# Kernel tuning notes

Measured on AMD Instinct MI355X. Metric: run time of the kernel, lower is better.

Reference implementation:

```python
import jax, jax.numpy as jnp
import numpy as np

N = 50000
E = 800000
IN = 128
HID = 32
OUT = 32
H1, H2 = 4, 4
NEG_SLOPE = 0.2


def setup_inputs() -> dict:
    key = jax.random.key(0)
    ks = jax.random.split(key, 12)
    x = jax.random.normal(ks[0], (N, IN), dtype=jnp.float32)
    src = jax.random.randint(ks[1], (E,), 0, N, dtype=jnp.int32)
    dst = jax.random.randint(ks[2], (E,), 0, N, dtype=jnp.int32)
    s = 0.1
    # layer 1: fc (IN -> H1*HID, no bias), attn vectors (H1, HID), bias (H1*HID,)
    W1 = jax.random.normal(ks[3], (IN, H1 * HID), dtype=jnp.float32) * s
    al1 = jax.random.normal(ks[4], (H1, HID), dtype=jnp.float32) * s
    ar1 = jax.random.normal(ks[5], (H1, HID), dtype=jnp.float32) * s
    b1 = jnp.zeros((H1 * HID,), dtype=jnp.float32)
    # layer 2: fc (H1*HID -> H2*OUT, no bias)
    W2 = jax.random.normal(ks[6], (H1 * HID, H2 * OUT), dtype=jnp.float32) * s
    al2 = jax.random.normal(ks[7], (H2, OUT), dtype=jnp.float32) * s
    ar2 = jax.random.normal(ks[8], (H2, OUT), dtype=jnp.float32) * s
    b2 = jnp.zeros((H2 * OUT,), dtype=jnp.float32)
    return {"x": x, "W1": W1, "al1": al1, "ar1": ar1, "b1": b1,
            "W2": W2, "al2": al2, "ar2": ar2, "b2": b2,
            "src": src, "dst": dst}


def _gat_layer(x, W, al, ar, b, src, dst, n, h, d):
    # feat_drop is identity (eval mode)
    feat = (x @ W).reshape(n, h, d)                       # [N,H,D]
    el = jnp.einsum('nhd,hd->nh', feat, al)               # [N,H]
    er = jnp.einsum('nhd,hd->nh', feat, ar)               # [N,H]
    e = jax.nn.leaky_relu(el[src] + er[dst], NEG_SLOPE)   # [E,H] SDDMM
    # edge softmax over incoming edges of each destination node
    emax = jax.ops.segment_max(e, dst, num_segments=n)    # [N,H]
    emax = jnp.where(jnp.isfinite(emax), emax, 0.0)       # guard 0-in-degree
    w = jnp.exp(e - emax[dst])                            # [E,H]
    denom = jax.ops.segment_sum(w, dst, num_segments=n)   # [N,H]
    alpha = w / jnp.maximum(denom[dst], 1e-9)             # [E,H]; attn_drop identity
    # SpMM aggregation
    rst = jax.ops.segment_sum(feat[src] * alpha[:, :, None], dst, num_segments=n)
    # residual: in_feats == h*d for both layers -> DGL uses Identity res_fc
    rst = rst + x.reshape(n, h, d)
    rst = rst + b.reshape(1, h, d)
    return rst


def reference(x, W1, al1, ar1, b1, W2, al2, ar2, b2, src, dst):
    h = _gat_layer(x, W1, al1, ar1, b1, src, dst, N, H1, HID)
    h = jax.nn.elu(h)                                     # layer-1 activation
    h = h.reshape(N, H1 * HID)                            # flatten(1)
    h = _gat_layer(h, W2, al2, ar2, b2, src, dst, N, H2, OUT)
    return h.mean(axis=1)                                 # [N,OUT]
```

## Files before the change

### kernel.cpp

```cpp
#include <hip/hip_runtime.h>
#include <cstdint>
#include <cstddef>

#define NEG_SLOPE 0.2f

typedef __bf16 bf16x8 __attribute__((ext_vector_type(8)));
typedef float  f32x4  __attribute__((ext_vector_type(4)));

__device__ inline unsigned int bf16pair(float a, float b) {
    unsigned int ua = __float_as_uint(a), ub = __float_as_uint(b);
    ua += 0x7fffu + ((ua >> 16) & 1u);
    ub += 0x7fffu + ((ub >> 16) & 1u);
    return (ua >> 16) | (ub & 0xffff0000u);
}
__device__ inline unsigned short bf16r(float x) {
    unsigned int u = __float_as_uint(x);
    u += 0x7fffu + ((u >> 16) & 1u);
    return (unsigned short)(u >> 16);
}

__global__ __launch_bounds__(256) void wtrans_kernel(
    const float* __restrict__ W1, const float* __restrict__ W2,
    unsigned short* __restrict__ Wt1, unsigned short* __restrict__ Wt2)
{
    __shared__ float tile[64][65];
    const float* W = (blockIdx.x < 4) ? W1 : W2;
    unsigned short* Wt = (blockIdx.x < 4) ? Wt1 : Wt2;
    const int tb = blockIdx.x & 3;
    const int k0 = (tb >> 1) * 64, n0 = (tb & 1) * 64;
    const int c = threadIdx.x & 63, r4 = threadIdx.x >> 6;
#pragma unroll
    for (int i = 0; i < 16; ++i) {
        const int r = i * 4 + r4;
        tile[r][c] = W[(size_t)(k0 + r) * 128 + n0 + c];
    }
    __syncthreads();
#pragma unroll
    for (int i = 0; i < 16; ++i) {
        const int nn = i * 4 + r4;
        Wt[(size_t)(n0 + nn) * 128 + k0 + c] = bf16r(tile[c][nn]);
    }
}

__global__ __launch_bounds__(256, 3) void gemm_attn_kernel(
    const float* __restrict__ X, const unsigned short* __restrict__ Wt,
    const float* __restrict__ al, const float* __restrict__ ar,
    unsigned short* __restrict__ feat16, float* __restrict__ el,
    float* __restrict__ er, int n)
{
    __shared__ unsigned short sX[64][136];
    __shared__ unsigned short sW[128][136];

    const int t = threadIdx.x;
    const int rowbase = blockIdx.x * 64;

#pragma unroll
    for (int i = 0; i < 8; ++i) {
        const int idx = t + 256 * i;
        const int row = idx >> 5;
        const int kq  = (idx & 31) * 4;
        int g = rowbase + row; if (g >= n) g = n - 1;
        const float4 v = *(const float4*)&X[(size_t)g * 128 + kq];
        uint2 pk;
        pk.x = bf16pair(v.x, v.y);
        pk.y = bf16pair(v.z, v.w);
        *(uint2*)&sX[row][kq] = pk;
    }
#pragma unroll
    for (int i = 0; i < 8; ++i) {
        const int idx = t + 256 * i;
        const int row = idx >> 4;
        const int q   = idx & 15;
        *(uint4*)&sW[row][q * 8] = *(const uint4*)&Wt[(size_t)row * 128 + q * 8];
    }
    __syncthreads();

    const int lane = t & 63;
    const int w    = t >> 6;
    const int m    = lane & 15;
    const int g4   = lane >> 4;

    bf16x8 a[4];
#pragma unroll
    for (int ks = 0; ks < 4; ++ks)
        a[ks] = *(const bf16x8*)&sX[w * 16 + m][ks * 32 + g4 * 8];

    float elacc[4][4] = {{0}}, eracc[4][4] = {{0}};
    unsigned short fout[8][4];

#pragma unroll
    for (int ct = 0; ct < 8; ct += 2) {
        f32x4 acc0 = {0.f, 0.f, 0.f, 0.f}, acc1 = {0.f, 0.f, 0.f, 0.f};
        const int n0 = ct * 16 + m, n1 = n0 + 16;
#pragma unroll
        for (int ks = 0; ks < 4; ++ks) {
            const bf16x8 b0 = *(const bf16x8*)&sW[n0][ks * 32 + g4 * 8];
            const bf16x8 b1 = *(const bf16x8*)&sW[n1][ks * 32 + g4 * 8];
            acc0 = __builtin_amdgcn_mfma_f32_16x16x32_bf16(a[ks], b0, acc0, 0, 0, 0);
            acc1 = __builtin_amdgcn_mfma_f32_16x16x32_bf16(a[ks], b1, acc1, 0, 0, 0);
        }
        const int h = ct >> 1;
        const float al0 = al[n0], ar0 = ar[n0];
        const float al1 = al[n1], ar1 = ar[n1];
#pragma unroll
        for (int r = 0; r < 4; ++r) {
            elacc[r][h] += acc0[r] * al0 + acc1[r] * al1;
            eracc[r][h] += acc0[r] * ar0 + acc1[r] * ar1;
            fout[ct][r]     = bf16r(acc0[r]);
            fout[ct + 1][r] = bf16r(acc1[r]);
        }
    }

    __syncthreads();
#pragma unroll
    for (int ct = 0; ct < 8; ++ct)
#pragma unroll
        for (int r = 0; r < 4; ++r)
            sX[w * 16 + g4 * 4 + r][(ct & 1) * 16 + (ct >> 1) * 32 + m] = fout[ct][r];
    __syncthreads();
    {
        const int row = t >> 2;
        const int q   = t & 3;
        const int g   = rowbase + row;
        if (g < n) {
#pragma unroll
            for (int i = 0; i < 4; ++i) {
                const int c0 = q * 8 + i * 32;
                *(uint4*)&feat16[(size_t)g * 128 + c0] = *(const uint4*)&sX[row][c0];
            }
        }
    }

#pragma unroll
    for (int r = 0; r < 4; ++r)
#pragma unroll
        for (int h = 0; h < 4; ++h) {
            float a_ = elacc[r][h], b_ = eracc[r][h];
            a_ += __shfl_xor(a_, 1); b_ += __shfl_xor(b_, 1);
            a_ += __shfl_xor(a_, 2); b_ += __shfl_xor(b_, 2);
            a_ += __shfl_xor(a_, 4); b_ += __shfl_xor(b_, 4);
            a_ += __shfl_xor(a_, 8); b_ += __shfl_xor(b_, 8);
            elacc[r][h] = a_; eracc[r][h] = b_;
        }
    if (m == 0) {
#pragma unroll
        for (int r = 0; r < 4; ++r) {
            const int row = rowbase + w * 16 + g4 * 4 + r;
            if (row < n) {
#pragma unroll
                for (int h = 0; h < 4; ++h) {
                    el[(size_t)row * 4 + h] = elacc[r][h];
                    er[(size_t)row * 4 + h] = eracc[r][h];
                }
            }
        }
    }
}


__global__ void rank_kernel(const int* __restrict__ dst, int* __restrict__ deg,
                            int* __restrict__ rank, int E)
{
    const int e4 = (blockIdx.x * blockDim.x + threadIdx.x) * 4;
    if (e4 + 4 <= E) {
        const int4 d = *(const int4*)&dst[e4];
        int4 r;
        r.x = atomicAdd(&deg[d.x], 1);
        r.y = atomicAdd(&deg[d.y], 1);
        r.z = atomicAdd(&deg[d.z], 1);
        r.w = atomicAdd(&deg[d.w], 1);
        *(int4*)&rank[e4] = r;
    } else {
        for (int e = e4; e < E; ++e) rank[e] = atomicAdd(&deg[dst[e]], 1);
    }
}

__global__ __launch_bounds__(1024) void scan_kernel(
    const int* __restrict__ deg, int* __restrict__ off, int n)
{
    __shared__ int wsums[16];
    __shared__ int s_carry;
    const int tid  = threadIdx.x;
    const int lane = tid & 63;
    const int wid  = tid >> 6;

    if (tid == 0) { s_carry = 0; off[0] = 0; }
    __syncthreads();

    const int n4 = n >> 2;
    const int4* __restrict__ deg4 = (const int4*)deg;

    for (int base = 0; base < n4; base += 1024) {
        const int i4 = base + tid;
        int4 v = make_int4(0, 0, 0, 0);
        if (i4 < n4) v = deg4[i4];
        const int t0 = v.x, t1 = t0 + v.y, t2 = t1 + v.z, t3 = t2 + v.w;

        int x = t3;
#pragma unroll
        for (int d = 1; d < 64; d <<= 1) {
            int y = __shfl_up(x, d);
            if (lane >= d) x += y;
        }
        if (lane == 63) wsums[wid] = x;
        __syncthreads();

        if (wid == 0 && lane < 16) {
            int xx = wsums[lane];
#pragma unroll
            for (int d = 1; d < 16; d <<= 1) {
                int y = __shfl_up(xx, d);
                if (lane >= d) xx += y;
            }
            wsums[lane] = xx;
        }
        __syncthreads();

        const int wp   = (wid == 0) ? 0 : wsums[wid - 1];
        const int excl = s_carry + wp + (x - t3);
        if (i4 < n4) {
            off[4 * i4 + 1] = excl + t0;
            off[4 * i4 + 2] = excl + t1;
            off[4 * i4 + 3] = excl + t2;
            off[4 * i4 + 4] = excl + t3;
        }
        __syncthreads();
        if (tid == 0) s_carry += wsums[15];
        __syncthreads();
    }
}

__global__ void place_kernel(const int* __restrict__ src, const int* __restrict__ dst,
                             const int* __restrict__ off, const int* __restrict__ rank,
                             int* __restrict__ csr_src, int E)
{
    const int e4 = (blockIdx.x * blockDim.x + threadIdx.x) * 4;
    if (e4 + 4 <= E) {
        const int4 s = *(const int4*)&src[e4];
        const int4 d = *(const int4*)&dst[e4];
        const int4 r = *(const int4*)&rank[e4];
        const int o0 = off[d.x], o1 = off[d.y], o2 = off[d.z], o3 = off[d.w];
        csr_src[o0 + r.x] = s.x;
        csr_src[o1 + r.y] = s.y;
        csr_src[o2 + r.z] = s.z;
        csr_src[o3 + r.w] = s.w;
    } else {
        for (int e = e4; e < E; ++e)
            csr_src[off[dst[e]] + rank[e]] = src[e];
    }
}

template <bool LAYER2>
__global__ __launch_bounds__(256) void agg_kernel(
    const int* __restrict__ off, const int* __restrict__ csr_src,
    const unsigned short* __restrict__ feat16, const float* __restrict__ el,
    const float* __restrict__ er, const float* __restrict__ resid,
    const float* __restrict__ bias, float* __restrict__ out, int n)
{
    const int lane = threadIdx.x & 63;
    const int node = blockIdx.x * 4 + (threadIdx.x >> 6);
    if (node >= n) return;

    const int h  = lane >> 4;
    const int d0 = 2 * lane;

    const float erh = er[(size_t)node * 4 + h];
    const unsigned int* __restrict__ fb = (const unsigned int*)feat16;

    const int beg = off[node], end = off[node + 1];

    float acc0 = 0.f, acc1 = 0.f, sw = 0.f;
    int j = beg;

#define EDGE4(J)                                                              \
    {                                                                         \
        const int s0 = csr_src[J], s1 = csr_src[(J) + 1];                     \
        const int s2 = csr_src[(J) + 2], s3 = csr_src[(J) + 3];               \
        const float e0 = el[(size_t)s0 * 4 + h];                              \
        const float e1 = el[(size_t)s1 * 4 + h];                              \
        const float e2 = el[(size_t)s2 * 4 + h];                              \
        const float e3 = el[(size_t)s3 * 4 + h];                              \
        const unsigned int u0 = fb[(size_t)s0 * 64 + lane];                   \
        const unsigned int u1 = fb[(size_t)s1 * 64 + lane];                   \
        const unsigned int u2 = fb[(size_t)s2 * 64 + lane];                   \
        const unsigned int u3 = fb[(size_t)s3 * 64 + lane];                   \
        float a0 = e0 + erh, a1 = e1 + erh, a2 = e2 + erh, a3 = e3 + erh;     \
        a0 = (a0 >= 0.f) ? a0 : NEG_SLOPE * a0;                               \
        a1 = (a1 >= 0.f) ? a1 : NEG_SLOPE * a1;                               \
        a2 = (a2 >= 0.f) ? a2 : NEG_SLOPE * a2;                               \
        a3 = (a3 >= 0.f) ? a3 : NEG_SLOPE * a3;                               \
        const float w0 = __expf(a0), w1 = __expf(a1);                         \
        const float w2 = __expf(a2), w3 = __expf(a3);                         \
        acc0 += w0 * __uint_as_float(u0 << 16);                               \
        acc1 += w0 * __uint_as_float(u0 & 0xffff0000u);                       \
        acc0 += w1 * __uint_as_float(u1 << 16);                               \
        acc1 += w1 * __uint_as_float(u1 & 0xffff0000u);                       \
        acc0 += w2 * __uint_as_float(u2 << 16);                               \
        acc1 += w2 * __uint_as_float(u2 & 0xffff0000u);                       \
        acc0 += w3 * __uint_as_float(u3 << 16);                               \
        acc1 += w3 * __uint_as_float(u3 & 0xffff0000u);                       \
        sw += w0 + w1 + w2 + w3;                                              \
    }

    for (; j + 8 <= end; j += 8) { EDGE4(j) EDGE4(j + 4) }
    for (; j + 4 <= end; j += 4) { EDGE4(j) }
#undef EDGE4
    for (; j < end; ++j) {
        const int s = csr_src[j];
        float e = el[(size_t)s * 4 + h] + erh;
        e = (e >= 0.f) ? e : NEG_SLOPE * e;
        const float w = __expf(e);
        const unsigned int u = fb[(size_t)s * 64 + lane];
        acc0 += w * __uint_as_float(u << 16);
        acc1 += w * __uint_as_float(u & 0xffff0000u);
        sw += w;
    }

    const float inv = 1.f / fmaxf(sw, 1e-9f);
    const float2 rs = *(const float2*)&resid[(size_t)node * 128 + d0];
    float v0 = acc0 * inv + rs.x + bias[d0];
    float v1 = acc1 * inv + rs.y + bias[d0 + 1];

    if (!LAYER2) {
        v0 = (v0 > 0.f) ? v0 : expm1f(v0);
        v1 = (v1 > 0.f) ? v1 : expm1f(v1);
        *(float2*)&out[(size_t)node * 128 + d0] = make_float2(v0, v1);
    } else {
        float s0 = v0, s1 = v1;
        s0 += __shfl_xor(s0, 16); s1 += __shfl_xor(s1, 16);
        s0 += __shfl_xor(s0, 32); s1 += __shfl_xor(s1, 32);
        if (lane < 16)
            *(float2*)&out[(size_t)node * 32 + 2 * lane] =
                make_float2(s0 * 0.25f, s1 * 0.25f);
    }
}

extern "C" void kernel_launch(void* const* d_in, const int* in_sizes, int n_in,
                              void* d_out, int out_size, void* d_ws, size_t ws_size,
                              hipStream_t stream)
{
    const float* x   = (const float*)d_in[0];
    const float* W1  = (const float*)d_in[1];
    const float* al1 = (const float*)d_in[2];
    const float* ar1 = (const float*)d_in[3];
    const float* b1  = (const float*)d_in[4];
    const float* W2  = (const float*)d_in[5];
    const float* al2 = (const float*)d_in[6];
    const float* ar2 = (const float*)d_in[7];
    const float* b2  = (const float*)d_in[8];
    const int*   src = (const int*)d_in[9];
    const int*   dst = (const int*)d_in[10];

    const int n = in_sizes[0] / 128;
    const int E = in_sizes[9];
    float* out = (float*)d_out;

    char* p = (char*)d_ws;
    float* h1    = (float*)p;          p += (size_t)n * 128 * sizeof(float);
    unsigned short* feat16 = (unsigned short*)p; p += (size_t)n * 128 * sizeof(unsigned short);
    float* el    = (float*)p;          p += (size_t)n * 4 * sizeof(float);
    float* er    = (float*)p;          p += (size_t)n * 4 * sizeof(float);
    int* off     = (int*)p;            p += (size_t)(n + 1) * sizeof(int);
    int* deg     = (int*)p;            p += (size_t)n * sizeof(int);
    int* rank    = (int*)p;            p += (size_t)E * sizeof(int);
    int* csr     = (int*)p;            p += (size_t)E * sizeof(int);
    unsigned short* wt1 = (unsigned short*)p; p += (size_t)128 * 128 * sizeof(unsigned short);
    unsigned short* wt2 = (unsigned short*)p; p += (size_t)128 * 128 * sizeof(unsigned short);

    hipMemsetAsync(deg, 0, (size_t)n * sizeof(int), stream);

    const int gemm_grid  = (n + 63) / 64;
    const int edge4_grid = (E / 4 + 255) / 256;
    const int agg_grid   = (n + 3) / 4;

    wtrans_kernel<<<8, 256, 0, stream>>>(W1, W2, wt1, wt2);
    gemm_attn_kernel<<<gemm_grid, 256, 0, stream>>>(x, wt1, al1, ar1, feat16, el, er, n);
    rank_kernel<<<edge4_grid, 256, 0, stream>>>(dst, deg, rank, E);
    scan_kernel<<<1, 1024, 0, stream>>>(deg, off, n);
    place_kernel<<<edge4_grid, 256, 0, stream>>>(src, dst, off, rank, csr, E);
    agg_kernel<false><<<agg_grid, 256, 0, stream>>>(off, csr, feat16, el, er, x, b1, h1, n);
    gemm_attn_kernel<<<gemm_grid, 256, 0, stream>>>(h1, wt2, al2, ar2, feat16, el, er, n);
    agg_kernel<true><<<agg_grid, 256, 0, stream>>>(off, csr, feat16, el, er, h1, b2, out, n);
}
```

Baseline: 270.1 us.

## Fuse degree-rank pass into layer-1 GEMM launch and deepen aggregation gather batching

```diff
diff --git a/kernel.cpp b/kernel.cpp
--- a/kernel.cpp
+++ b/kernel.cpp
@@ -42,16 +42,37 @@
     }
 }
 
+template <bool RANK>
 __global__ __launch_bounds__(256, 3) void gemm_attn_kernel(
     const float* __restrict__ X, const unsigned short* __restrict__ Wt,
     const float* __restrict__ al, const float* __restrict__ ar,
     unsigned short* __restrict__ feat16, float* __restrict__ el,
-    float* __restrict__ er, int n)
+    float* __restrict__ er, int n, int gemm_blocks,
+    const int* __restrict__ dst, int* __restrict__ deg,
+    int* __restrict__ rank, int E)
 {
     __shared__ unsigned short sX[64][136];
     __shared__ unsigned short sW[128][136];
 
     const int t = threadIdx.x;
+
+    if (RANK && (int)blockIdx.x >= gemm_blocks) {
+        const int bid = blockIdx.x - gemm_blocks;
+        const int e4 = (bid * 256 + t) * 4;
+        if (e4 + 4 <= E) {
+            const int4 d = *(const int4*)&dst[e4];
+            int4 r;
+            r.x = atomicAdd(&deg[d.x], 1);
+            r.y = atomicAdd(&deg[d.y], 1);
+            r.z = atomicAdd(&deg[d.z], 1);
+            r.w = atomicAdd(&deg[d.w], 1);
+            *(int4*)&rank[e4] = r;
+        } else {
+            for (int e = e4; e < E; ++e) rank[e] = atomicAdd(&deg[dst[e]], 1);
+        }
+        return;
+    }
+
     const int rowbase = blockIdx.x * 64;
 
 #pragma unroll
@@ -116,7 +137,7 @@
     for (int ct = 0; ct < 8; ++ct)
 #pragma unroll
         for (int r = 0; r < 4; ++r)
-            sX[w * 16 + g4 * 4 + r][(ct & 1) * 16 + (ct >> 1) * 32 + m] = fout[ct][r];
+            sX[w * 16 + g4 * 4 + r][ct * 16 + m] = fout[ct][r];
     __syncthreads();
     {
         const int row = t >> 2;
@@ -154,24 +175,6 @@
                 }
             }
         }
-    }
-}
-
-
-__global__ void rank_kernel(const int* __restrict__ dst, int* __restrict__ deg,
-                            int* __restrict__ rank, int E)
-{
-    const int e4 = (blockIdx.x * blockDim.x + threadIdx.x) * 4;
-    if (e4 + 4 <= E) {
-        const int4 d = *(const int4*)&dst[e4];
-        int4 r;
-        r.x = atomicAdd(&deg[d.x], 1);
-        r.y = atomicAdd(&deg[d.y], 1);
-        r.z = atomicAdd(&deg[d.z], 1);
-        r.w = atomicAdd(&deg[d.w], 1);
-        *(int4*)&rank[e4] = r;
-    } else {
-        for (int e = e4; e < E; ++e) rank[e] = atomicAdd(&deg[dst[e]], 1);
     }
 }
 
@@ -251,7 +254,7 @@
 }
 
 template <bool LAYER2>
-__global__ __launch_bounds__(256) void agg_kernel(
+__global__ __launch_bounds__(256, 4) void agg_kernel(
     const int* __restrict__ off, const int* __restrict__ csr_src,
     const unsigned short* __restrict__ feat16, const float* __restrict__ el,
     const float* __restrict__ er, const float* __restrict__ resid,
@@ -272,48 +275,51 @@
     float acc0 = 0.f, acc1 = 0.f, sw = 0.f;
     int j = beg;
 
-#define EDGE4(J)                                                              \
-    {                                                                         \
-        const int s0 = csr_src[J], s1 = csr_src[(J) + 1];                     \
-        const int s2 = csr_src[(J) + 2], s3 = csr_src[(J) + 3];               \
-        const float e0 = el[(size_t)s0 * 4 + h];                              \
-        const float e1 = el[(size_t)s1 * 4 + h];                              \
-        const float e2 = el[(size_t)s2 * 4 + h];                              \
-        const float e3 = el[(size_t)s3 * 4 + h];                              \
-        const unsigned int u0 = fb[(size_t)s0 * 64 + lane];                   \
-        const unsigned int u1 = fb[(size_t)s1 * 64 + lane];                   \
-        const unsigned int u2 = fb[(size_t)s2 * 64 + lane];                   \
-        const unsigned int u3 = fb[(size_t)s3 * 64 + lane];                   \
-        float a0 = e0 + erh, a1 = e1 + erh, a2 = e2 + erh, a3 = e3 + erh;     \
-        a0 = (a0 >= 0.f) ? a0 : NEG_SLOPE * a0;                               \
-        a1 = (a1 >= 0.f) ? a1 : NEG_SLOPE * a1;                               \
-        a2 = (a2 >= 0.f) ? a2 : NEG_SLOPE * a2;                               \
-        a3 = (a3 >= 0.f) ? a3 : NEG_SLOPE * a3;                               \
-        const float w0 = __expf(a0), w1 = __expf(a1);                         \
-        const float w2 = __expf(a2), w3 = __expf(a3);                         \
-        acc0 += w0 * __uint_as_float(u0 << 16);                               \
-        acc1 += w0 * __uint_as_float(u0 & 0xffff0000u);                       \
-        acc0 += w1 * __uint_as_float(u1 << 16);                               \
-        acc1 += w1 * __uint_as_float(u1 & 0xffff0000u);                       \
-        acc0 += w2 * __uint_as_float(u2 << 16);                               \
-        acc1 += w2 * __uint_as_float(u2 & 0xffff0000u);                       \
-        acc0 += w3 * __uint_as_float(u3 << 16);                               \
-        acc1 += w3 * __uint_as_float(u3 & 0xffff0000u);                       \
-        sw += w0 + w1 + w2 + w3;                                              \
-    }
-
-    for (; j + 8 <= end; j += 8) { EDGE4(j) EDGE4(j + 4) }
-    for (; j + 4 <= end; j += 4) { EDGE4(j) }
-#undef EDGE4
+    for (; j + 16 <= end; j += 16) {
+        int s[16]; float ev[16]; unsigned int uv[16];
+#pragma unroll
+        for (int q = 0; q < 16; ++q) s[q] = csr_src[j + q];
+#pragma unroll
+        for (int q = 0; q < 16; ++q) ev[q] = el[(size_t)s[q] * 4 + h];
+#pragma unroll
+        for (int q = 0; q < 16; ++q) uv[q] = fb[(size_t)s[q] * 64 + lane];
+#pragma unroll
+        for (int q = 0; q < 16; ++q) {
+            float a = ev[q] + erh;
+            a = fmaxf(a, NEG_SLOPE * a);
+            const float wq = __expf(a);
+            acc0 += wq * __uint_as_float(uv[q] << 16);
+            acc1 += wq * __uint_as_float(uv[q] & 0xffff0000u);
+            sw += wq;
+        }
+    }
+    for (; j + 4 <= end; j += 4) {
+        int s[4]; float ev[4]; unsigned int uv[4];
+#pragma unroll
+        for (int q = 0; q < 4; ++q) s[q] = csr_src[j + q];
+#pragma unroll
+        for (int q = 0; q < 4; ++q) ev[q] = el[(size_t)s[q] * 4 + h];
+#pragma unroll
+        for (int q = 0; q < 4; ++q) uv[q] = fb[(size_t)s[q] * 64 + lane];
+#pragma unroll
+        for (int q = 0; q < 4; ++q) {
+            float a = ev[q] + erh;
+            a = fmaxf(a, NEG_SLOPE * a);
+            const float wq = __expf(a);
+            acc0 += wq * __uint_as_float(uv[q] << 16);
+            acc1 += wq * __uint_as_float(uv[q] & 0xffff0000u);
+            sw += wq;
+        }
+    }
     for (; j < end; ++j) {
         const int s = csr_src[j];
-        float e = el[(size_t)s * 4 + h] + erh;
-        e = (e >= 0.f) ? e : NEG_SLOPE * e;
-        const float w = __expf(e);
+        float a = el[(size_t)s * 4 + h] + erh;
+        a = fmaxf(a, NEG_SLOPE * a);
+        const float wq = __expf(a);
         const unsigned int u = fb[(size_t)s * 64 + lane];
-        acc0 += w * __uint_as_float(u << 16);
-        acc1 += w * __uint_as_float(u & 0xffff0000u);
-        sw += w;
+        acc0 += wq * __uint_as_float(u << 16);
+        acc1 += wq * __uint_as_float(u & 0xffff0000u);
+        sw += wq;
     }
 
     const float inv = 1.f / fmaxf(sw, 1e-9f);
@@ -374,11 +380,12 @@
     const int agg_grid   = (n + 3) / 4;
 
     wtrans_kernel<<<8, 256, 0, stream>>>(W1, W2, wt1, wt2);
-    gemm_attn_kernel<<<gemm_grid, 256, 0, stream>>>(x, wt1, al1, ar1, feat16, el, er, n);
-    rank_kernel<<<edge4_grid, 256, 0, stream>>>(dst, deg, rank, E);
+    gemm_attn_kernel<true><<<gemm_grid + edge4_grid, 256, 0, stream>>>(
+        x, wt1, al1, ar1, feat16, el, er, n, gemm_grid, dst, deg, rank, E);
     scan_kernel<<<1, 1024, 0, stream>>>(deg, off, n);
     place_kernel<<<edge4_grid, 256, 0, stream>>>(src, dst, off, rank, csr, E);
     agg_kernel<false><<<agg_grid, 256, 0, stream>>>(off, csr, feat16, el, er, x, b1, h1, n);
-    gemm_attn_kernel<<<gemm_grid, 256, 0, stream>>>(h1, wt2, al2, ar2, feat16, el, er, n);
+    gemm_attn_kernel<false><<<gemm_grid, 256, 0, stream>>>(
+        h1, wt2, al2, ar2, feat16, el, er, n, gemm_grid, nullptr, nullptr, nullptr, 0);
     agg_kernel<true><<<agg_grid, 256, 0, stream>>>(off, csr, feat16, el, er, h1, b2, out, n);
 }
```

New measurement: 274.0 us. About the same (+1.4%).
